# Performance work log

Hardware: AMD Instinct MI355X
Metric: run time of the kernel (lower is better)

The kernel has to match this reference:

```python
import jax, jax.numpy as jnp
import numpy as np

N_HEAD = 16
D_HEAD = 64
D_MODEL = 1024
SCALE = 1.0 / D_HEAD ** 0.5


def setup_inputs() -> dict:
    key = jax.random.key(0)
    k1, k2 = jax.random.split(key)
    h = jax.random.normal(k1, (2048, 2, D_MODEL), dtype=jnp.float32)
    # torch Linear weight layout: [out_features, in_features]
    w_qkv = jax.random.normal(k2, (3 * N_HEAD * D_HEAD, D_MODEL), dtype=jnp.float32) * (D_MODEL ** -0.5)
    return {"h": h, "w_qkv": w_qkv}


def reference(h, w_qkv):
    qlen, bsz, _ = h.shape
    heads = h @ w_qkv.T  # [qlen, bsz, 3*n_head*d_head]
    head_q, head_k, head_v = jnp.split(heads, 3, axis=-1)
    head_q = head_q.reshape(qlen, bsz, N_HEAD, D_HEAD)
    head_k = head_k.reshape(qlen, bsz, N_HEAD, D_HEAD)
    head_v = head_v.reshape(qlen, bsz, N_HEAD, D_HEAD)
    attn_score = jnp.einsum('ibnd,jbnd->ijbn', head_q, head_k) * SCALE
    attn_prob = jax.nn.softmax(attn_score, axis=1)  # softmax over key dim j
    # dropout is identity at p=0.0 / eval mode
    attn_vec = jnp.einsum('ijbn,jbnd->ibnd', attn_prob, head_v)
    attn_vec = attn_vec.reshape(qlen, bsz, N_HEAD * D_HEAD)
    return attn_vec, attn_prob
```

## Files before the change

### kernel.cpp

```cpp
#include <hip/hip_runtime.h>

typedef _Float16 f16;
typedef f16 f16x8 __attribute__((ext_vector_type(8)));
typedef f16 f16x4 __attribute__((ext_vector_type(4)));
typedef float f32x4 __attribute__((ext_vector_type(4)));

#define QLEN 2048
#define BSZ 2
#define NH 16
#define DH 64
#define DM 1024
#define NBN (BSZ*NH)
#define SCALE 0.125f

static __device__ __forceinline__ f32x4 mfma16(f16x8 a, f16x8 b, f32x4 c) {
  return __builtin_amdgcn_mfma_f32_16x16x32_f16(a, b, c, 0, 0, 0);
}

static __device__ __forceinline__ void gload_lds16(const void* g, void* l) {
  __builtin_amdgcn_global_load_lds((const __attribute__((address_space(1))) unsigned int*)g,
                                   (__attribute__((address_space(3))) unsigned int*)l,
                                   16, 0, 0);
}

static __device__ __forceinline__ void barrier_lds() {
  __builtin_amdgcn_sched_barrier(0);
  asm volatile("s_waitcnt lgkmcnt(0)" ::: "memory");
  __builtin_amdgcn_s_barrier();
  __builtin_amdgcn_sched_barrier(0);
}

__global__ __launch_bounds__(256) void cvt_f32_f16(const float* __restrict__ s,
                                                   f16* __restrict__ d, int n4) {
  int idx = blockIdx.x * 256 + threadIdx.x;
  if (idx >= n4) return;
  f32x4 v = ((const f32x4*)s)[idx];
  f16x4 o;
#pragma unroll
  for (int q = 0; q < 4; ++q) o[q] = (f16)v[q];
  ((f16x4*)d)[idx] = o;
}

__global__ __launch_bounds__(256) void qkv_gemm(const f16* __restrict__ A, const f16* __restrict__ W,
                                                f16* __restrict__ Qs, f16* __restrict__ Ks,
                                                f16* __restrict__ Vt) {
  __shared__ f16 As[128 * 32];
  __shared__ f16 Bs[128 * 32];
  const int bid = blockIdx.x;
  const int r0 = (bid & 31) << 7;
  const int c0 = (bid >> 5) << 7;
  const int t = threadIdx.x;
  const int lane = t & 63, w = t >> 6;
  const int wr = (w >> 1) << 6, wc = (w & 1) << 6;
  const int l15 = lane & 15, lhi = lane >> 4;

  f32x4 acc[4][4] = {};

  const f16* ga = A + (size_t)(r0 + (t >> 2)) * DM + ((t & 3) << 3);
  const f16* gb = W + (size_t)(c0 + (t >> 2)) * DM + ((t & 3) << 3);
  char* la = (char*)As + w * 1024;
  char* lb = (char*)Bs + w * 1024;

  for (int k0 = 0; k0 < DM; k0 += 32) {
    __syncthreads();
    gload_lds16(ga + k0, la);
    gload_lds16(ga + k0 + (size_t)64 * DM, la + 4096);
    gload_lds16(gb + k0, lb);
    gload_lds16(gb + k0 + (size_t)64 * DM, lb + 4096);
    __syncthreads();
    f16x8 af[4], bf[4];
#pragma unroll
    for (int m = 0; m < 4; ++m)
      af[m] = *(const f16x8*)&As[(wr + m * 16 + l15) * 32 + lhi * 8];
#pragma unroll
    for (int n = 0; n < 4; ++n)
      bf[n] = *(const f16x8*)&Bs[(wc + n * 16 + l15) * 32 + lhi * 8];
#pragma unroll
    for (int m = 0; m < 4; ++m)
#pragma unroll
      for (int n = 0; n < 4; ++n)
        acc[m][n] = mfma16(af[m], bf[n], acc[m][n]);
  }

  const int part = c0 >> 10;
#pragma unroll
  for (int m = 0; m < 4; ++m) {
#pragma unroll
    for (int n = 0; n < 4; ++n) {
#pragma unroll
      for (int q = 0; q < 4; ++q) {
        int r = r0 + wr + m * 16 + lhi * 4 + q;
        int c = c0 + wc + n * 16 + l15;
        int i = r >> 1, b = r & 1;
        int nh = (c >> 6) & 15, d = c & 63;
        int bn = b * 16 + nh;
        f16 v = (f16)acc[m][n][q];
        if (part == 0)       Qs[((size_t)bn * QLEN + i) * DH + d] = v;
        else if (part == 1)  Ks[((size_t)bn * QLEN + i) * DH + d] = v;
        else                 Vt[((size_t)bn * DH + d) * QLEN + i] = v;
      }
    }
  }
}

__global__ __launch_bounds__(256) void flash_attn(const f16* __restrict__ Qs, const f16* __restrict__ Ks,
                                                  const f16* __restrict__ Vt, float* __restrict__ av,
                                                  float* __restrict__ sm, float* __restrict__ srl) {
  __shared__ f16 plds[4][16 * 32];
  const int bid = blockIdx.x;
  const int bn = bid >> 4, ib = bid & 15;
  const int t = threadIdx.x, lane = t & 63, w = t >> 6;
  const int l15 = lane & 15, lhi = lane >> 4;
  const int i0 = (ib << 7) + (w << 5);
  const f16* Qb = Qs + ((size_t)bn << 17);
  const f16* Kb = Ks + ((size_t)bn << 17);
  const f16* Vb = Vt + ((size_t)bn << 17);
  f16* pw = plds[w];

  f16x8 qf[2][2];
#pragma unroll
  for (int rg = 0; rg < 2; ++rg)
#pragma unroll
    for (int kc = 0; kc < 2; ++kc)
      qf[rg][kc] = *(const f16x8*)&Qb[(size_t)(i0 + rg * 16 + l15) * DH + kc * 32 + lhi * 8];

  f32x4 o[2][4] = {};
  float mrun[2][4], lrun[2][4];
#pragma unroll
  for (int rg = 0; rg < 2; ++rg)
#pragma unroll
    for (int q = 0; q < 4; ++q) { mrun[rg][q] = -1e30f; lrun[rg][q] = 0.f; }

  for (int j0 = 0; j0 < QLEN; j0 += 32) {
    f16x8 kf[2][2], vf[4];
#pragma unroll
    for (int jc = 0; jc < 2; ++jc)
#pragma unroll
      for (int kc = 0; kc < 2; ++kc)
        kf[jc][kc] = *(const f16x8*)&Kb[(size_t)(j0 + jc * 16 + l15) * DH + kc * 32 + lhi * 8];
#pragma unroll
    for (int dc = 0; dc < 4; ++dc)
      vf[dc] = *(const f16x8*)&Vb[(size_t)(dc * 16 + l15) * QLEN + j0 + lhi * 8];

#pragma unroll
    for (int rg = 0; rg < 2; ++rg) {
      f32x4 s[2];
#pragma unroll
      for (int jc = 0; jc < 2; ++jc) {
        f32x4 z = {0.f, 0.f, 0.f, 0.f};
        z = mfma16(qf[rg][0], kf[jc][0], z);
        z = mfma16(qf[rg][1], kf[jc][1], z);
        s[jc] = z;
      }
      float p[2][4], alpha[4];
#pragma unroll
      for (int q = 0; q < 4; ++q) {
        float v0 = s[0][q] * SCALE, v1 = s[1][q] * SCALE;
        float tm = fmaxf(v0, v1);
        tm = fmaxf(tm, __shfl_xor(tm, 1));
        tm = fmaxf(tm, __shfl_xor(tm, 2));
        tm = fmaxf(tm, __shfl_xor(tm, 4));
        tm = fmaxf(tm, __shfl_xor(tm, 8));
        float mnew = fmaxf(mrun[rg][q], tm);
        alpha[q] = __expf(mrun[rg][q] - mnew);
        mrun[rg][q] = mnew;
        p[0][q] = __expf(v0 - mnew);
        p[1][q] = __expf(v1 - mnew);
        float r = p[0][q] + p[1][q];
        r += __shfl_xor(r, 1);
        r += __shfl_xor(r, 2);
        r += __shfl_xor(r, 4);
        r += __shfl_xor(r, 8);
        lrun[rg][q] = lrun[rg][q] * alpha[q] + r;
      }
#pragma unroll
      for (int dc = 0; dc < 4; ++dc)
#pragma unroll
        for (int q = 0; q < 4; ++q)
          o[rg][dc][q] *= alpha[q];
#pragma unroll
      for (int jc = 0; jc < 2; ++jc)
#pragma unroll
        for (int q = 0; q < 4; ++q)
          pw[(lhi * 4 + q) * 32 + jc * 16 + l15] = (f16)p[jc][q];
      f16x8 pa = *(const f16x8*)&pw[l15 * 32 + lhi * 8];
#pragma unroll
      for (int dc = 0; dc < 4; ++dc)
        o[rg][dc] = mfma16(pa, vf[dc], o[rg][dc]);
    }
  }

  const int b = bn >> 4, nh = bn & 15;
#pragma unroll
  for (int rg = 0; rg < 2; ++rg)
#pragma unroll
    for (int dc = 0; dc < 4; ++dc)
#pragma unroll
      for (int q = 0; q < 4; ++q) {
        int i = i0 + rg * 16 + lhi * 4 + q;
        av[((size_t)i * BSZ + b) * (NH * DH) + nh * DH + dc * 16 + l15] =
            o[rg][dc][q] / lrun[rg][q];
      }
  if (l15 == 0) {
#pragma unroll
    for (int rg = 0; rg < 2; ++rg)
#pragma unroll
      for (int q = 0; q < 4; ++q) {
        int i = i0 + rg * 16 + lhi * 4 + q;
        sm[bn * QLEN + i] = mrun[rg][q];
        srl[bn * QLEN + i] = 1.0f / lrun[rg][q];
      }
  }
}

#define LOADK(buf, chn)                                                        \
  do {                                                                         \
    _Pragma("unroll") for (int bl_ = 0; bl_ < 4; ++bl_) {                      \
      const f16* Kb_ = Ks + (((size_t)(w4 + bl_)) << 17) +                     \
                       (size_t)(j0 + (chn) * 16 + l15) * DH + lhi * 8;         \
      buf[bl_][0] = *(const f16x8*)(Kb_);                                      \
      buf[bl_][1] = *(const f16x8*)(Kb_ + 32);                                 \
    }                                                                          \
  } while (0)

#define SUBCHUNK(cur, nxt, ch, sub)                                            \
  do {                                                                         \
    f16 stv[4][4];                                                             \
    _Pragma("unroll") for (int bl_ = 0; bl_ < 4; ++bl_) {                      \
      f32x4 z = {0.f, 0.f, 0.f, 0.f};                                          \
      z = mfma16(qf[bl_][0], cur[bl_][0], z);                                  \
      z = mfma16(qf[bl_][1], cur[bl_][1], z);                                  \
      _Pragma("unroll") for (int q_ = 0; q_ < 4; ++q_)                         \
        stv[bl_][q_] = (f16)(__expf(z[q_] * SCALE - mm[bl_][q_]) * rl[bl_][q_]); \
    }                                                                          \
    __builtin_amdgcn_sched_barrier(0);                                         \
    { const int nch_ = ((ch) + 1 < 16) ? (ch) + 1 : 15; LOADK(nxt, nch_); }    \
    __builtin_amdgcn_sched_barrier(0);                                         \
    _Pragma("unroll") for (int q_ = 0; q_ < 4; ++q_) {                         \
      const int i_l = lhi * 4 + q_;                                            \
      const int jl = (sub) * 16 + l15;                                         \
      f16x4 v = {stv[0][q_], stv[1][q_], stv[2][q_], stv[3][q_]};              \
      *(f16x4*)&tile[(i_l * 64 + jl) * 32 + ((w ^ (l15 & 7)) << 2)] = v;       \
    }                                                                          \
  } while (0)

__global__ __launch_bounds__(512, 1) void write_probs(const f16* __restrict__ Qs, const f16* __restrict__ Ks,
                                                      const float* __restrict__ sm, const float* __restrict__ srl,
                                                      float* __restrict__ pout) {
  __shared__ f16 tile[16 * 64 * 32];
  const int bid = blockIdx.x;
  const int it = bid >> 3, jt = bid & 7;
  const int i0 = it << 4, j0 = jt << 8;
  const int t = threadIdx.x, lane = t & 63, w = t >> 6;
  const int l15 = lane & 15, lhi = lane >> 4;
  const int w4 = w * 4;

  f16x8 qf[4][2];
  float mm[4][4], rl[4][4];
#pragma unroll
  for (int bl = 0; bl < 4; ++bl) {
    const int bn = w4 + bl;
    const f16* Qb = Qs + ((size_t)bn << 17);
#pragma unroll
    for (int kc = 0; kc < 2; ++kc)
      qf[bl][kc] = *(const f16x8*)&Qb[(size_t)(i0 + l15) * DH + kc * 32 + lhi * 8];
#pragma unroll
    for (int q = 0; q < 4; ++q) {
      const int i = i0 + lhi * 4 + q;
      mm[bl][q] = sm[bn * QLEN + i];
      rl[bl][q] = srl[bn * QLEN + i];
    }
  }

  const int j_s = t >> 3;
  const int o = t & 7;
  const int swz = o ^ (j_s & 7);

  f16x8 kfA[4][2], kfB[4][2];
  LOADK(kfA, 0);

  for (int ph = 0; ph < 4; ++ph) {
    const int c0 = ph * 4;
    SUBCHUNK(kfA, kfB, c0 + 0, 0);
    SUBCHUNK(kfB, kfA, c0 + 1, 1);
    SUBCHUNK(kfA, kfB, c0 + 2, 2);
    SUBCHUNK(kfB, kfA, c0 + 3, 3);
    barrier_lds();
#pragma unroll
    for (int r = 0; r < 16; ++r) {
      f16x4 v = *(const f16x4*)&tile[(r * 64 + j_s) * 32 + (swz << 2)];
      f32x4 ov = {(float)v[0], (float)v[1], (float)v[2], (float)v[3]};
      float* op = pout + ((size_t)(i0 + r) * QLEN + j0 + ph * 64 + j_s) * NBN + o * 4;
      *(f32x4*)op = ov;
    }
    barrier_lds();
  }
}

extern "C" void kernel_launch(void* const* d_in, const int* in_sizes, int n_in,
                              void* d_out, int out_size, void* d_ws, size_t ws_size,
                              hipStream_t stream) {
  const float* h  = (const float*)d_in[0];
  const float* wq = (const float*)d_in[1];
  float* av   = (float*)d_out;
  float* pout = av + (size_t)QLEN * BSZ * NH * DH;

  char* ws = (char*)d_ws;
  f16* hh  = (f16*)ws;
  f16* wh  = (f16*)(ws + (8u << 20));
  f16* Qsc = (f16*)(ws + (16u << 20));
  f16* Ksc = (f16*)(ws + (24u << 20));
  f16* Vtc = (f16*)(ws + (32u << 20));
  float* smv  = (float*)(ws + (40u << 20));
  float* srlv = (float*)(ws + (40u << 20) + (QLEN * NBN * 4));

  const int nh4 = QLEN * BSZ * DM / 4;
  const int nw4 = 3 * NH * DH * DM / 4;
  cvt_f32_f16<<<nh4 / 256, 256, 0, stream>>>(h, hh, nh4);
  cvt_f32_f16<<<nw4 / 256, 256, 0, stream>>>(wq, wh, nw4);
  qkv_gemm<<<32 * 24, 256, 0, stream>>>(hh, wh, Qsc, Ksc, Vtc);
  flash_attn<<<NBN * 16, 256, 0, stream>>>(Qsc, Ksc, Vtc, av, smv, srlv);
  write_probs<<<128 * 8, 512, 0, stream>>>(Qsc, Ksc, smv, srlv, pout);
}
```

Before: 360.7 us.

## Restructure write_probs: 8-row tiles over full key range with double-buffered LDS

Each write_probs block now handles 8 query rows across all 2048 keys instead of 16 rows by 256 keys, giving 256 blocks that loop over 32 phases. The LDS tile is double-buffered so the second barrier per phase goes away, and the probability output uses nontemporal stores. Launch bounds now allow two blocks per CU. In exchange, the 16-row MFMA computes half-wasted rows: only lanes with lhi<2 write, so half the QK compute is discarded. The grid is also smaller, which could hurt load balance on a large GPU.

```diff
diff --git a/kernel.cpp b/kernel.cpp
--- a/kernel.cpp
+++ b/kernel.cpp
@@ -213,17 +213,17 @@
   }
 }
 
-#define LOADK(buf, chn)                                                        \
+#define LOADK(buf, c)                                                          \
   do {                                                                         \
     _Pragma("unroll") for (int bl_ = 0; bl_ < 4; ++bl_) {                      \
       const f16* Kb_ = Ks + (((size_t)(w4 + bl_)) << 17) +                     \
-                       (size_t)(j0 + (chn) * 16 + l15) * DH + lhi * 8;         \
+                       (size_t)((c) * 16 + l15) * DH + lhi * 8;                \
       buf[bl_][0] = *(const f16x8*)(Kb_);                                      \
       buf[bl_][1] = *(const f16x8*)(Kb_ + 32);                                 \
     }                                                                          \
   } while (0)
 
-#define SUBCHUNK(cur, nxt, ch, sub)                                            \
+#define SUBCHUNK(cur, nxt, c, sub, tb)                                         \
   do {                                                                         \
     f16 stv[4][4];                                                             \
     _Pragma("unroll") for (int bl_ = 0; bl_ < 4; ++bl_) {                      \
@@ -234,23 +234,24 @@
         stv[bl_][q_] = (f16)(__expf(z[q_] * SCALE - mm[bl_][q_]) * rl[bl_][q_]); \
     }                                                                          \
     __builtin_amdgcn_sched_barrier(0);                                         \
-    { const int nch_ = ((ch) + 1 < 16) ? (ch) + 1 : 15; LOADK(nxt, nch_); }    \
+    { const int nc_ = ((c) + 1 < 128) ? (c) + 1 : 127; LOADK(nxt, nc_); }      \
     __builtin_amdgcn_sched_barrier(0);                                         \
-    _Pragma("unroll") for (int q_ = 0; q_ < 4; ++q_) {                         \
-      const int i_l = lhi * 4 + q_;                                            \
-      const int jl = (sub) * 16 + l15;                                         \
-      f16x4 v = {stv[0][q_], stv[1][q_], stv[2][q_], stv[3][q_]};              \
-      *(f16x4*)&tile[(i_l * 64 + jl) * 32 + ((w ^ (l15 & 7)) << 2)] = v;       \
+    if (lhi < 2) {                                                             \
+      _Pragma("unroll") for (int q_ = 0; q_ < 4; ++q_) {                       \
+        const int i_l = lhi * 4 + q_;                                          \
+        const int jl = (sub) * 16 + l15;                                       \
+        f16x4 v = {stv[0][q_], stv[1][q_], stv[2][q_], stv[3][q_]};            \
+        *(f16x4*)&(tb)[(i_l * 64 + jl) * 32 + ((w ^ (jl & 7)) << 2)] = v;      \
+      }                                                                        \
     }                                                                          \
   } while (0)
 
-__global__ __launch_bounds__(512, 1) void write_probs(const f16* __restrict__ Qs, const f16* __restrict__ Ks,
+__global__ __launch_bounds__(512, 2) void write_probs(const f16* __restrict__ Qs, const f16* __restrict__ Ks,
                                                       const float* __restrict__ sm, const float* __restrict__ srl,
                                                       float* __restrict__ pout) {
-  __shared__ f16 tile[16 * 64 * 32];
+  __shared__ f16 tile[2][8 * 64 * 32];
   const int bid = blockIdx.x;
-  const int it = bid >> 3, jt = bid & 7;
-  const int i0 = it << 4, j0 = jt << 8;
+  const int i0 = bid << 3;
   const int t = threadIdx.x, lane = t & 63, w = t >> 6;
   const int l15 = lane & 15, lhi = lane >> 4;
   const int w4 = w * 4;
@@ -263,37 +264,41 @@
     const f16* Qb = Qs + ((size_t)bn << 17);
 #pragma unroll
     for (int kc = 0; kc < 2; ++kc)
-      qf[bl][kc] = *(const f16x8*)&Qb[(size_t)(i0 + l15) * DH + kc * 32 + lhi * 8];
+      qf[bl][kc] = *(const f16x8*)&Qb[(size_t)(i0 + (l15 & 7)) * DH + kc * 32 + lhi * 8];
 #pragma unroll
     for (int q = 0; q < 4; ++q) {
-      const int i = i0 + lhi * 4 + q;
+      const int i = i0 + ((lhi * 4 + q) & 7);
       mm[bl][q] = sm[bn * QLEN + i];
       rl[bl][q] = srl[bn * QLEN + i];
     }
   }
 
-  const int j_s = t >> 3;
+  const int i_r = t >> 6;
+  const int jo = (t >> 3) & 7;
   const int o = t & 7;
-  const int swz = o ^ (j_s & 7);
 
   f16x8 kfA[4][2], kfB[4][2];
   LOADK(kfA, 0);
 
-  for (int ph = 0; ph < 4; ++ph) {
-    const int c0 = ph * 4;
-    SUBCHUNK(kfA, kfB, c0 + 0, 0);
-    SUBCHUNK(kfB, kfA, c0 + 1, 1);
-    SUBCHUNK(kfA, kfB, c0 + 2, 2);
-    SUBCHUNK(kfB, kfA, c0 + 3, 3);
+  for (int ph = 0; ph < 32; ++ph) {
+    f16* tb = tile[ph & 1];
+    const int jbase = ph << 6;
+    const int c0 = ph << 2;
+    SUBCHUNK(kfA, kfB, c0 + 0, 0, tb);
+    SUBCHUNK(kfB, kfA, c0 + 1, 1, tb);
+    SUBCHUNK(kfA, kfB, c0 + 2, 2, tb);
+    SUBCHUNK(kfB, kfA, c0 + 3, 3, tb);
     barrier_lds();
-#pragma unroll
-    for (int r = 0; r < 16; ++r) {
-      f16x4 v = *(const f16x4*)&tile[(r * 64 + j_s) * 32 + (swz << 2)];
+
+#pragma unroll
+    for (int p = 0; p < 8; ++p) {
+      const int j_s = p * 8 + jo;
+      const int swz = o ^ (j_s & 7);
+      f16x4 v = *(const f16x4*)&tb[(i_r * 64 + j_s) * 32 + (swz << 2)];
       f32x4 ov = {(float)v[0], (float)v[1], (float)v[2], (float)v[3]};
-      float* op = pout + ((size_t)(i0 + r) * QLEN + j0 + ph * 64 + j_s) * NBN + o * 4;
-      *(f32x4*)op = ov;
+      float* op = pout + ((size_t)(i0 + i_r) * QLEN + jbase + j_s) * NBN + o * 4;
+      __builtin_nontemporal_store(ov, (f32x4*)op);
     }
-    barrier_lds();
   }
 }
 
@@ -320,5 +325,5 @@
   cvt_f32_f16<<<nw4 / 256, 256, 0, stream>>>(wq, wh, nw4);
   qkv_gemm<<<32 * 24, 256, 0, stream>>>(hh, wh, Qsc, Ksc, Vtc);
   flash_attn<<<NBN * 16, 256, 0, stream>>>(Qsc, Ksc, Vtc, av, smv, srlv);
-  write_probs<<<128 * 8, 512, 0, stream>>>(Qsc, Ksc, smv, srlv, pout);
-}
+  write_probs<<<256, 512, 0, stream>>>(Qsc, Ksc, smv, srlv, pout);
+}
```

Result: slower. 442.6 us (+22.7%).
